# Performance work log

Measured on AMD Instinct MI355X. Metric: run time of the kernel, lower is better.

Reference implementation:

```python
import jax, jax.numpy as jnp
import numpy as np

B, IN_DIM, OUT_DIM, MV = 8192, 256, 256, 8


def setup_inputs() -> dict:
    key = jax.random.key(0)
    k1, k2 = jax.random.split(key)
    x = jax.random.normal(k1, (B, IN_DIM, MV), dtype=jnp.float32)
    weights = jax.random.normal(k2, (IN_DIM, OUT_DIM, MV), dtype=jnp.float32) * 0.01
    bias = jnp.zeros((OUT_DIM, MV), dtype=jnp.float32)
    return {"x": x, "weights": weights, "bias": bias}


def reference(x, weights, bias):
    # Simplified GA-3D geometric product, summed over in_dim (j), per out_dim (i):
    #   y[..., i, 0] = sum_j x[..., j, 0]*W[j,i,0] + x[..., j, 1]*W[j,i,1] + x[..., j, 2]*W[j,i,2]
    #   y[..., i, 4] = sum_j x[..., j, 1]*W[j,i,2] - x[..., j, 2]*W[j,i,1] + x[..., j, 4]*W[j,i,0]
    #   all other multivector components receive only the bias.
    # Scalar component: dot over first 3 multivector slots.
    c0 = jnp.einsum('bjk,jik->bi', x[..., 0:3], weights[..., 0:3])  # (B, OUT_DIM)
    # Bivector component e23: x1*w2 - x2*w1 + x4*w0.
    xv = jnp.stack([x[..., 1], -x[..., 2], x[..., 4]], axis=-1)          # (B, IN_DIM, 3)
    wv = jnp.stack([weights[..., 2], weights[..., 1], weights[..., 0]], axis=-1)  # (IN_DIM, OUT_DIM, 3)
    c4 = jnp.einsum('bjk,jik->bi', xv, wv)  # (B, OUT_DIM)
    y = jnp.broadcast_to(bias, (x.shape[0],) + bias.shape)  # (B, OUT_DIM, MV)
    y = y.at[..., 0].add(c0).at[..., 4].add(c4)
    return y
```

## Files before the change

### kernel.cpp

```cpp
#include <hip/hip_runtime.h>
#include <hip/hip_bf16.h>

typedef __attribute__((ext_vector_type(4))) float f32x4;
typedef __attribute__((ext_vector_type(8))) short bf16x8;
typedef __attribute__((ext_vector_type(4))) short short4v;

#define ACH 1032
#define AB_BYTES 66048
#define CS 516

__device__ __forceinline__ short f2bf(float f) {
  __hip_bfloat16 h = __float2bfloat16(f);
  return __builtin_bit_cast(short, h);
}

#define GLD_LDS16(gp, lp)                                                    \
  __builtin_amdgcn_global_load_lds(                                          \
      (const __attribute__((address_space(1))) unsigned int*)(gp),           \
      (__attribute__((address_space(3))) unsigned int*)(lp), 16, 0, 0)

#define WAITV(N)                                            \
  {                                                         \
    asm volatile("s_waitcnt vmcnt(" #N ")" ::: "memory");   \
    __builtin_amdgcn_sched_barrier(0);                      \
  }
#define QBAR()                                              \
  {                                                         \
    asm volatile("s_waitcnt lgkmcnt(0)" ::: "memory");      \
    __builtin_amdgcn_sched_barrier(0);                      \
    __builtin_amdgcn_s_barrier();                           \
    __builtin_amdgcn_sched_barrier(0);                      \
  }

__global__ __launch_bounds__(256) void ga_prep_B(const float* __restrict__ W,
                                                 short* __restrict__ Bp) {
  const int gid = blockIdx.x * 256 + threadIdx.x;
  const int l  = gid & 63;
  const int cg = (gid >> 6) & 31;
  const int it = gid >> 11;
  const int ln = l & 15, q = l >> 4;
  const int hc = cg >> 4;
  const int i  = (cg & 15) * 16 + ln;
  const int j0 = it * 8 + q * 2;
  const float4* W4 = (const float4*)W;

  bf16x8 o;
#pragma unroll
  for (int jj = 0; jj < 2; ++jj) {
    const float4 wv = W4[((j0 + jj) * 256 + i) * 2];
    if (!hc) {
      o[jj * 4 + 0] = f2bf(wv.x); o[jj * 4 + 1] = f2bf(wv.y);
      o[jj * 4 + 2] = f2bf(wv.z); o[jj * 4 + 3] = 0;
    } else {
      o[jj * 4 + 0] = 0;           o[jj * 4 + 1] = f2bf(wv.z);
      o[jj * 4 + 2] = f2bf(-wv.y); o[jj * 4 + 3] = f2bf(wv.x);
    }
  }
  *(bf16x8*)&Bp[(size_t)gid * 8] = o;
}

__global__ __launch_bounds__(1024, 4) void ga_mv_main(
    const float* __restrict__ x, const short* __restrict__ Bp,
    const float* __restrict__ bias, float* __restrict__ y) {
  __shared__ __align__(16) char smem[131584];
  short* Ab = (short*)smem;
  short* Bs = (short*)(smem + AB_BYTES);
  float* c_lds = (float*)(smem + AB_BYTES);

  const int t = threadIdx.x;
  const int lane = t & 63, w = t >> 6;
  const int ln = lane & 15, qq = lane >> 4;
  const int R0 = blockIdx.x * 32;

  const float* xsrc = x + (size_t)(R0 + (t >> 5)) * 2048 + (t & 31) * 8;
  const int crow = t >> 5, cj = t & 31;
  f32x4 xA0, xA1, xB0, xB1;

#define XLOAD(g)                                                \
  {                                                             \
    const f32x4* p = (const f32x4*)(xsrc + (g) * 256);          \
    if ((g) & 1) { xB0 = p[0]; xB1 = p[1]; }                    \
    else         { xA0 = p[0]; xA1 = p[1]; }                    \
  }

#define CONV(g)                                                 \
  {                                                             \
    const f32x4 v0 = ((g) & 1) ? xB0 : xA0;                     \
    const f32x4 v1 = ((g) & 1) ? xB1 : xA1;                     \
    short4v a;                                                  \
    a[0] = f2bf(v0[0]); a[1] = f2bf(v0[1]);                     \
    a[2] = f2bf(v0[2]); a[3] = f2bf(v1[0]);                     \
    *(short4v*)&Ab[crow * ACH + (32 * (g) + cj) * 4] = a;       \
  }

  const int boff = w * 1024 + lane * 8;
#define BDMA(s)                                                 \
  {                                                             \
    const short* gp = Bp + (size_t)(s) * 16384 + boff;          \
    short* lp = Bs + ((s) & 1) * 16384 + boff;                  \
    GLD_LDS16(gp, lp);                                          \
    GLD_LDS16(gp + 512, lp + 512);                              \
  }

  f32x4 acc[2][2] = {};

#define ITER(it, N)                                                           \
  {                                                                           \
    WAITV(N);                               \
    const bf16x8 af0 = *(const bf16x8*)&Ab[ln * ACH + (it) * 32 + qq * 8];    \
    const bf16x8 af1 =                                                        \
        *(const bf16x8*)&Ab[(16 + ln) * ACH + (it) * 32 + qq * 8];            \
    const bf16x8 bf0 = *(const bf16x8*)&Bs[((it) & 1) * 16384 + boff];        \
    const bf16x8 bf1 = *(const bf16x8*)&Bs[((it) & 1) * 16384 + boff + 512];  \
    acc[0][0] = __builtin_amdgcn_mfma_f32_16x16x32_bf16(af0, bf0, acc[0][0],  \
                                                        0, 0, 0);             \
    acc[1][0] = __builtin_amdgcn_mfma_f32_16x16x32_bf16(af1, bf0, acc[1][0],  \
                                                        0, 0, 0);             \
    acc[0][1] = __builtin_amdgcn_mfma_f32_16x16x32_bf16(af0, bf1, acc[0][1],  \
                                                        0, 0, 0);             \
    acc[1][1] = __builtin_amdgcn_mfma_f32_16x16x32_bf16(af1, bf1, acc[1][1],  \
                                                        0, 0, 0);             \
    __builtin_amdgcn_sched_barrier(0);  \
    if ((it) + 2 < 32) BDMA((it) + 2);                                        \
  }

#define BATCH(g, DOX, NT3)         \
  {                                \
    CONV(g);                       \
    QBAR();                        \
    ITER(4 * (g) + 0, 2)           \
    ITER(4 * (g) + 1, 2)           \
    if (DOX) XLOAD((g) + 2);       \
    ITER(4 * (g) + 2, 2)           \
    ITER(4 * (g) + 3, NT3)         \
  }

  BDMA(0);
  BDMA(1);
  XLOAD(0);
  XLOAD(1);

  BATCH(0, 1, 2) BATCH(1, 1, 2) BATCH(2, 1, 2) BATCH(3, 1, 2)
  BATCH(4, 1, 2) BATCH(5, 1, 2) BATCH(6, 0, 2) BATCH(7, 0, 0)

  QBAR();

  const int h = t & 1, p = (t >> 1) & 255, rh = t >> 9;
  const float4 bv = ((const float4*)bias)[p * 2 + h];
  f32x4* y4 = (f32x4*)y;

#pragma unroll
  for (int ep = 0; ep < 2; ++ep) {
    if (ep) QBAR();
#pragma unroll
    for (int n = 0; n < 2; ++n)
#pragma unroll
      for (int r = 0; r < 4; ++r)
        c_lds[(qq * 4 + r) * CS + w * 32 + n * 16 + ln] = acc[ep][n][r];
    QBAR();
#pragma unroll
    for (int rr = 0; rr < 8; ++rr) {
      const int row = rr * 2 + rh;
      f32x4 o;
      o[0] = bv.x; o[1] = bv.y; o[2] = bv.z; o[3] = bv.w;
      o[0] += c_lds[row * CS + h * 256 + p];
      __builtin_nontemporal_store(
          o, &y4[((size_t)(R0 + ep * 16 + row) * 256 + p) * 2 + h]);
    }
  }
}

extern "C" void kernel_launch(void* const* d_in, const int* in_sizes, int n_in,
                              void* d_out, int out_size, void* d_ws, size_t ws_size,
                              hipStream_t stream) {
  const float* x = (const float*)d_in[0];
  const float* W = (const float*)d_in[1];
  const float* bias = (const float*)d_in[2];
  float* y = (float*)d_out;
  short* Bp = (short*)d_ws;

  ga_prep_B<<<dim3(256), dim3(256), 0, stream>>>(W, Bp);
  ga_mv_main<<<dim3(256), dim3(1024), 0, stream>>>(x, Bp, bias, y);
}
```

Baseline: 131.3 us.

## Derive bivector B fragment in registers and load B directly from global

The prepacked weight buffer now holds only the scalar-component fragment; the bivector fragment is rebuilt in registers per iteration by bit shuffles and a sign flip on the bf16 lanes. B fragments are loaded straight from global into a 4-deep register ring instead of DMA'd into LDS with vmcnt waits, which halves LDS use and halves the prep kernel's work and the B traffic. The cost is extra VALU ops per MFMA step and relying on L2 for B reuse across waves, plus register pressure from the ring.

```diff
diff --git a/kernel.cpp b/kernel.cpp
--- a/kernel.cpp
+++ b/kernel.cpp
@@ -2,6 +2,7 @@
 #include <hip/hip_bf16.h>
 
 typedef __attribute__((ext_vector_type(4))) float f32x4;
+typedef __attribute__((ext_vector_type(4))) unsigned int u32x4;
 typedef __attribute__((ext_vector_type(8))) short bf16x8;
 typedef __attribute__((ext_vector_type(4))) short short4v;
 
@@ -14,16 +15,6 @@
   return __builtin_bit_cast(short, h);
 }
 
-#define GLD_LDS16(gp, lp)                                                    \
-  __builtin_amdgcn_global_load_lds(                                          \
-      (const __attribute__((address_space(1))) unsigned int*)(gp),           \
-      (__attribute__((address_space(3))) unsigned int*)(lp), 16, 0, 0)
-
-#define WAITV(N)                                            \
-  {                                                         \
-    asm volatile("s_waitcnt vmcnt(" #N ")" ::: "memory");   \
-    __builtin_amdgcn_sched_barrier(0);                      \
-  }
 #define QBAR()                                              \
   {                                                         \
     asm volatile("s_waitcnt lgkmcnt(0)" ::: "memory");      \
@@ -36,11 +27,10 @@
                                                  short* __restrict__ Bp) {
   const int gid = blockIdx.x * 256 + threadIdx.x;
   const int l  = gid & 63;
-  const int cg = (gid >> 6) & 31;
-  const int it = gid >> 11;
+  const int cg = (gid >> 6) & 15;
+  const int it = gid >> 10;
   const int ln = l & 15, q = l >> 4;
-  const int hc = cg >> 4;
-  const int i  = (cg & 15) * 16 + ln;
+  const int i  = cg * 16 + ln;
   const int j0 = it * 8 + q * 2;
   const float4* W4 = (const float4*)W;
 
@@ -48,13 +38,8 @@
 #pragma unroll
   for (int jj = 0; jj < 2; ++jj) {
     const float4 wv = W4[((j0 + jj) * 256 + i) * 2];
-    if (!hc) {
-      o[jj * 4 + 0] = f2bf(wv.x); o[jj * 4 + 1] = f2bf(wv.y);
-      o[jj * 4 + 2] = f2bf(wv.z); o[jj * 4 + 3] = 0;
-    } else {
-      o[jj * 4 + 0] = 0;           o[jj * 4 + 1] = f2bf(wv.z);
-      o[jj * 4 + 2] = f2bf(-wv.y); o[jj * 4 + 3] = f2bf(wv.x);
-    }
+    o[jj * 4 + 0] = f2bf(wv.x); o[jj * 4 + 1] = f2bf(wv.y);
+    o[jj * 4 + 2] = f2bf(wv.z); o[jj * 4 + 3] = 0;
   }
   *(bf16x8*)&Bp[(size_t)gid * 8] = o;
 }
@@ -62,10 +47,9 @@
 __global__ __launch_bounds__(1024, 4) void ga_mv_main(
     const float* __restrict__ x, const short* __restrict__ Bp,
     const float* __restrict__ bias, float* __restrict__ y) {
-  __shared__ __align__(16) char smem[131584];
+  __shared__ __align__(16) char smem[AB_BYTES];
   short* Ab = (short*)smem;
-  short* Bs = (short*)(smem + AB_BYTES);
-  float* c_lds = (float*)(smem + AB_BYTES);
+  float* c_lds = (float*)smem;
 
   const int t = threadIdx.x;
   const int lane = t & 63, w = t >> 6;
@@ -93,55 +77,53 @@
     *(short4v*)&Ab[crow * ACH + (32 * (g) + cj) * 4] = a;       \
   }
 
-  const int boff = w * 1024 + lane * 8;
-#define BDMA(s)                                                 \
-  {                                                             \
-    const short* gp = Bp + (size_t)(s) * 16384 + boff;          \
-    short* lp = Bs + ((s) & 1) * 16384 + boff;                  \
-    GLD_LDS16(gp, lp);                                          \
-    GLD_LDS16(gp + 512, lp + 512);                              \
-  }
+  const size_t bbase = (size_t)w * 512 + lane * 8;
+  bf16x8 Bf[4];
+#define LB(itv, b) { Bf[b] = *(const bf16x8*)(Bp + (size_t)(itv) * 8192 + bbase); }
 
   f32x4 acc[2][2] = {};
 
-#define ITER(it, N)                                                           \
+#define ITER(it)                                                              \
   {                                                                           \
-    WAITV(N);                               \
     const bf16x8 af0 = *(const bf16x8*)&Ab[ln * ACH + (it) * 32 + qq * 8];    \
     const bf16x8 af1 =                                                        \
         *(const bf16x8*)&Ab[(16 + ln) * ACH + (it) * 32 + qq * 8];            \
-    const bf16x8 bf0 = *(const bf16x8*)&Bs[((it) & 1) * 16384 + boff];        \
-    const bf16x8 bf1 = *(const bf16x8*)&Bs[((it) & 1) * 16384 + boff + 512];  \
-    acc[0][0] = __builtin_amdgcn_mfma_f32_16x16x32_bf16(af0, bf0, acc[0][0],  \
+    const bf16x8 F = Bf[(it) & 3];                                            \
+    const u32x4 fu = __builtin_bit_cast(u32x4, F);                            \
+    u32x4 gu;                                                                 \
+    gu.x = fu.y << 16;                                    \
+    gu.y = ((fu.x >> 16) | (fu.x << 16)) ^ 0x8000u;       \
+    gu.z = fu.w << 16;                                                        \
+    gu.w = ((fu.z >> 16) | (fu.z << 16)) ^ 0x8000u;                           \
+    const bf16x8 G = __builtin_bit_cast(bf16x8, gu);                          \
+    acc[0][0] = __builtin_amdgcn_mfma_f32_16x16x32_bf16(af0, F, acc[0][0],    \
                                                         0, 0, 0);             \
-    acc[1][0] = __builtin_amdgcn_mfma_f32_16x16x32_bf16(af1, bf0, acc[1][0],  \
+    acc[1][0] = __builtin_amdgcn_mfma_f32_16x16x32_bf16(af1, F, acc[1][0],    \
                                                         0, 0, 0);             \
-    acc[0][1] = __builtin_amdgcn_mfma_f32_16x16x32_bf16(af0, bf1, acc[0][1],  \
+    acc[0][1] = __builtin_amdgcn_mfma_f32_16x16x32_bf16(af0, G, acc[0][1],    \
                                                         0, 0, 0);             \
-    acc[1][1] = __builtin_amdgcn_mfma_f32_16x16x32_bf16(af1, bf1, acc[1][1],  \
+    acc[1][1] = __builtin_amdgcn_mfma_f32_16x16x32_bf16(af1, G, acc[1][1],    \
                                                         0, 0, 0);             \
-    __builtin_amdgcn_sched_barrier(0);  \
-    if ((it) + 2 < 32) BDMA((it) + 2);                                        \
+    if ((it) + 4 < 32) LB((it) + 4, (it) & 3);                                \
   }
 
-#define BATCH(g, DOX, NT3)         \
+#define BATCH(g, DOX)              \
   {                                \
     CONV(g);                       \
     QBAR();                        \
-    ITER(4 * (g) + 0, 2)           \
-    ITER(4 * (g) + 1, 2)           \
+    ITER(4 * (g) + 0)              \
+    ITER(4 * (g) + 1)              \
     if (DOX) XLOAD((g) + 2);       \
-    ITER(4 * (g) + 2, 2)           \
-    ITER(4 * (g) + 3, NT3)         \
+    ITER(4 * (g) + 2)              \
+    ITER(4 * (g) + 3)              \
   }
 
-  BDMA(0);
-  BDMA(1);
+  LB(0, 0); LB(1, 1); LB(2, 2); LB(3, 3);
   XLOAD(0);
   XLOAD(1);
 
-  BATCH(0, 1, 2) BATCH(1, 1, 2) BATCH(2, 1, 2) BATCH(3, 1, 2)
-  BATCH(4, 1, 2) BATCH(5, 1, 2) BATCH(6, 0, 2) BATCH(7, 0, 0)
+  BATCH(0, 1) BATCH(1, 1) BATCH(2, 1) BATCH(3, 1)
+  BATCH(4, 1) BATCH(5, 1) BATCH(6, 0) BATCH(7, 0)
 
   QBAR();
 
@@ -156,7 +138,7 @@
     for (int n = 0; n < 2; ++n)
 #pragma unroll
       for (int r = 0; r < 4; ++r)
-        c_lds[(qq * 4 + r) * CS + w * 32 + n * 16 + ln] = acc[ep][n][r];
+        c_lds[(qq * 4 + r) * CS + n * 256 + w * 16 + ln] = acc[ep][n][r];
     QBAR();
 #pragma unroll
     for (int rr = 0; rr < 8; ++rr) {
@@ -179,6 +161,6 @@
   float* y = (float*)d_out;
   short* Bp = (short*)d_ws;
 
-  ga_prep_B<<<dim3(256), dim3(256), 0, stream>>>(W, Bp);
+  ga_prep_B<<<dim3(128), dim3(256), 0, stream>>>(W, Bp);
   ga_mv_main<<<dim3(256), dim3(1024), 0, stream>>>(x, Bp, bias, y);
 }
```

Measured after the change: 125.9 us. -4.1%, faster.
